# Kernel optimization log

Measured on AMD Instinct MI355X. Metric: run time of the kernel, lower is better.

Reference implementation:

```python
import jax, jax.numpy as jnp
import numpy as np

H, D = 8, 16
HD = H * D
SCALE0 = float(1.0 / np.sqrt(D * 1))   # degree-0 dot-product scale (order m=1)
SCALE1 = float(1.0 / np.sqrt(D * 3))   # degree-1 dot-product scale (order m=3)
SHARED = float(np.sqrt(0.5))           # shared_scale = sqrt(1/2) for DOT_PROD + SHARED
NEG = -1e9


def _split_heads_q(x):  # (b,n,HD,m) -> (b,H,n,D,m)
    b, n, _, m = x.shape
    return x.reshape(b, n, H, D, m).transpose(0, 2, 1, 3, 4)


def _split_heads_k(x):  # (b,n,N,HD,m) -> (b,H,n,N,D,m)
    b, n, N, _, m = x.shape
    return x.reshape(b, n, N, H, D, m).transpose(0, 3, 1, 2, 4, 5)


def _augment_kv(k, v, feats, W_self, null_k, null_v):
    # attend_self: VNLinear self key/value; use_null_kv: learned null tokens.
    b, n = feats.shape[:2]
    m = feats.shape[-1]
    skv = jnp.einsum('oc,bncm->bnom', W_self, feats)          # (b,n,2HD,m)
    sk, sv = jnp.split(skv, 2, axis=-2)
    sk = _split_heads_q(sk)[:, :, :, None]                     # (b,H,n,1,D,m)
    sv = _split_heads_q(sv)[:, :, :, None]
    nk = jnp.broadcast_to(null_k[None, :, None, None], (b, H, n, 1, D, m))
    nv = jnp.broadcast_to(null_v[None, :, None, None], (b, H, n, 1, D, m))
    k = jnp.concatenate([nk, sk, k], axis=3)                   # (b,H,n,2+N,D,m)
    v = jnp.concatenate([nv, sv, v], axis=3)
    return k, v


def _merge_heads(x):  # (b,H,n,D,m) -> (b,n,HD,m)
    b, _, n, _, m = x.shape
    return x.transpose(0, 2, 1, 3, 4).reshape(b, n, HD, m)


def _forward(q0, k0, v0, q1, k1, v1, feats0, feats1, edges,
             W_self_kv0, W_self_kv1, W_bias, self_bias, null_bias,
             null_k0, null_v0, null_k1, null_v1, head_weights1,
             W_out0, W_out1, neighbor_mask):
    b, n, N = edges.shape[:3]
    q0h, k0h, v0h = _split_heads_q(q0), _split_heads_k(k0), _split_heads_k(v0)
    q1h, k1h, v1h = _split_heads_q(q1), _split_heads_k(k1), _split_heads_k(v1)
    k0h, v0h = _augment_kv(k0h, v0h, feats0, W_self_kv0, null_k0, null_v0)
    k1h, v1h = _augment_kv(k1h, v1h, feats1, W_self_kv1, null_k1, null_v1)

    # pair bias for degree 0 (to_order==1); prepend null/self bias columns
    edge_bias = jnp.einsum('bnje,he->bhnj', edges, W_bias)     # (b,H,n,N)
    nb = jnp.broadcast_to(null_bias[None, :, None, None], (b, H, n, 1))
    sb = jnp.broadcast_to(self_bias[None, :, None, None], (b, H, n, 1))
    bias = jnp.concatenate([nb, sb, edge_bias], axis=-1)        # (b,H,n,2+N)

    sim0 = jnp.einsum('bhndm,bhnjdm->bhnj', q0h, k0h) * SCALE0 + bias
    w1 = jax.nn.softplus(head_weights1)                         # (1,H,1,1)
    sim1 = jnp.einsum('bhndm,bhnjdm->bhnj', q1h, k1h) * (SCALE1 * w1)

    total = (sim0 + sim1) * SHARED
    mask = jnp.concatenate(
        [jnp.ones((b, 1, n, 2), dtype=bool),                    # null + self always valid
         neighbor_mask[:, None]], axis=-1)
    total = jnp.where(mask, total, NEG)
    attn = jax.nn.softmax(total, axis=-1)                       # shared across degrees

    out0 = _merge_heads(jnp.einsum('bhnj,bhnjdm->bhndm', attn, v0h))
    out1 = _merge_heads(jnp.einsum('bhnj,bhnjdm->bhndm', attn, v1h))

    y0 = jnp.einsum('oc,bncm->bnom', W_out0, out0)              # FiberLinear deg 0
    y1 = jnp.einsum('oc,bncm->bnom', W_out1, out1)              # FiberLinear deg 1
    return y0, y1


def setup_inputs() -> dict:
    key = jax.random.key(0)
    ks = jax.random.split(key, 20)
    b, n, N, e = 1, 2048, 32, 32
    d0, d1 = 128, 64
    f = lambda k, s: jax.random.normal(k, s, dtype=jnp.float32) * 0.1
    return {
        'q0': f(ks[0], (b, n, HD, 1)), 'k0': f(ks[1], (b, n, N, HD, 1)), 'v0': f(ks[2], (b, n, N, HD, 1)),
        'q1': f(ks[3], (b, n, HD, 3)), 'k1': f(ks[4], (b, n, N, HD, 3)), 'v1': f(ks[5], (b, n, N, HD, 3)),
        'feats0': f(ks[6], (b, n, d0, 1)), 'feats1': f(ks[7], (b, n, d1, 3)),
        'edges': f(ks[8], (b, n, N, e)),
        'W_self_kv0': f(ks[9], (2 * HD, d0)), 'W_self_kv1': f(ks[10], (2 * HD, d1)),
        'W_bias': f(ks[11], (H, e)),
        'self_bias': jnp.zeros((H,), jnp.float32), 'null_bias': jnp.zeros((H,), jnp.float32),
        'null_k0': jnp.zeros((H, D, 1), jnp.float32), 'null_v0': jnp.zeros((H, D, 1), jnp.float32),
        'null_k1': jnp.zeros((H, D, 3), jnp.float32), 'null_v1': jnp.zeros((H, D, 3), jnp.float32),
        'head_weights1': jnp.full((1, H, 1, 1), float(np.log(np.e - 1.0)), jnp.float32),
        'W_out0': f(ks[12], (d0, HD)), 'W_out1': f(ks[13], (d1, HD)),
        'neighbor_mask': jax.random.uniform(ks[14], (b, n, N)) > 0.1,
    }


def reference(q0, k0, v0, q1, k1, v1, feats0, feats1, edges,
              W_self_kv0, W_self_kv1, W_bias, self_bias, null_bias,
              null_k0, null_v0, null_k1, null_v1, head_weights1,
              W_out0, W_out1, neighbor_mask):
    return _forward(q0, k0, v0, q1, k1, v1, feats0, feats1, edges,
                    W_self_kv0, W_self_kv1, W_bias, self_bias, null_bias,
                    null_k0, null_v0, null_k1, null_v1, head_weights1,
                    W_out0, W_out1, neighbor_mask)
```

## Files before the change

### kernel.cpp

```cpp
#include <hip/hip_runtime.h>

constexpr int kH  = 8;
constexpr int kD  = 16;
constexpr int kHD = 128;
constexpr int kN  = 32;
constexpr int kE  = 32;
constexpr int kD0 = 128;
constexpr int kD1 = 64;
constexpr int kPos = 2;

constexpr float SCALE0   = 0.25f;
constexpr float SCALE1   = 0.14433756729740643f;
constexpr float SHARED_S = 0.70710678118654752f;
constexpr float NEGV     = -1e9f;

__global__ __launch_bounds__(256, 4) void se3_fused(
    const float* __restrict__ q0, const float* __restrict__ q1,
    const float* __restrict__ k0, const float* __restrict__ k1,
    const float* __restrict__ v0, const float* __restrict__ v1,
    const float* __restrict__ feats0, const float* __restrict__ feats1,
    const float* __restrict__ edges,
    const float* __restrict__ Wskv0, const float* __restrict__ Wskv1,
    const float* __restrict__ Wbias,
    const float* __restrict__ sbias, const float* __restrict__ nbias,
    const float* __restrict__ nk0, const float* __restrict__ nk1,
    const float* __restrict__ nv0, const float* __restrict__ nv1,
    const float* __restrict__ hw1,
    const float* __restrict__ Wout0, const float* __restrict__ Wout1,
    const int* __restrict__ nmask,
    float* __restrict__ out, int n_total)
{
  const int i0 = blockIdx.x * kPos;
  const int t  = threadIdx.x;

  __shared__ __align__(16) float f0s[kPos][kD0];
  __shared__ __align__(16) float f1s[kPos][kD1 * 3];
  __shared__ __align__(16) float q0s[kPos][kHD];
  __shared__ __align__(16) float q1s[kPos][kHD * 3];
  __shared__ float edg[kPos][kN * (kE + 1)];
  __shared__ float wbs[kH * kE];
  __shared__ float w1s[kH];
  __shared__ int   nmL[kPos][kN];
  __shared__ float sk0[kPos][kHD];
  __shared__ __align__(16) float sk1[kPos][kHD * 3];
  __shared__ __align__(16) float sv0[kPos][kHD];
  __shared__ __align__(16) float sv1[kPos][kHD * 3];
  __shared__ float sc[kPos][kH][36];
  __shared__ __align__(16) float o0[kPos][kHD];
  __shared__ __align__(16) float o1[kPos][kHD * 3];

  if (t < kPos * 32) { int p = t >> 5, r = t & 31;
    ((float4*)f0s[p])[r] = ((const float4*)(feats0 + (size_t)(i0 + p) * kD0))[r]; }
  else if (t < kPos * 32 + kPos * 48) { int u = t - kPos * 32, p = u / 48, r = u % 48;
    ((float4*)f1s[p])[r] = ((const float4*)(feats1 + (size_t)(i0 + p) * kD1 * 3))[r]; }
  if (t >= 160 && t < 160 + kPos * 32) { int u = t - 160, p = u >> 5, r = u & 31;
    ((float4*)q0s[p])[r] = ((const float4*)(q0 + (size_t)(i0 + p) * kHD))[r]; }
  {
    int u = t; if (u < kPos * 96) { int p = u / 96, r = u % 96;
      ((float4*)q1s[p])[r] = ((const float4*)(q1 + (size_t)(i0 + p) * kHD * 3))[r]; }
  }
  for (int u = t; u < kPos * 256; u += 256) { int p = u >> 8, r = u & 255;
    float4 v = ((const float4*)(edges + (size_t)(i0 + p) * kN * kE))[r];
    int j = r >> 3, e4 = (r & 7) * 4;
    float* dst = &edg[p][j * 33 + e4];
    dst[0] = v.x; dst[1] = v.y; dst[2] = v.z; dst[3] = v.w; }
  if (t < kH * kE) wbs[t] = Wbias[t];
  if (t < kH) w1s[t] = log1pf(expf(hw1[t]));
  if (t < kPos * kN) { int p = t >> 5, j = t & 31;
    nmL[p][j] = nmask[(size_t)(i0 + p) * kN + j]; }
  __syncthreads();

  const int q4 = t & 3;
  const int qg = t >> 2;

  #pragma unroll
  for (int pass = 0; pass < 4; ++pass) {
    const int r = qg + 64 * pass;
    const float4* w0r = (const float4*)(Wskv0 + (size_t)r * kD0);
    float a0[kPos] = {};
    #pragma unroll
    for (int g = 0; g < 8; ++g) {
      float4 w = w0r[q4 + 4 * g]; int c = (q4 + 4 * g) * 4;
      #pragma unroll
      for (int p = 0; p < kPos; ++p)
        a0[p] += w.x * f0s[p][c] + w.y * f0s[p][c + 1]
               + w.z * f0s[p][c + 2] + w.w * f0s[p][c + 3];
    }
    const float4* w1r = (const float4*)(Wskv1 + (size_t)r * kD1);
    float a1[kPos][3] = {};
    #pragma unroll
    for (int g = 0; g < 4; ++g) {
      float4 w = w1r[q4 + 4 * g]; int c = (q4 + 4 * g) * 4;
      float wv[4] = {w.x, w.y, w.z, w.w};
      #pragma unroll
      for (int k = 0; k < 4; ++k) {
        #pragma unroll
        for (int p = 0; p < kPos; ++p) {
          const float* fp = &f1s[p][(c + k) * 3];
          a1[p][0] += wv[k] * fp[0];
          a1[p][1] += wv[k] * fp[1];
          a1[p][2] += wv[k] * fp[2];
        }
      }
    }
    #pragma unroll
    for (int p = 0; p < kPos; ++p) {
      a0[p] += __shfl_xor(a0[p], 1); a0[p] += __shfl_xor(a0[p], 2);
      #pragma unroll
      for (int c = 0; c < 3; ++c) {
        a1[p][c] += __shfl_xor(a1[p][c], 1);
        a1[p][c] += __shfl_xor(a1[p][c], 2);
      }
    }
    if (q4 == 0) {
      if (r < kHD) {
        #pragma unroll
        for (int p = 0; p < kPos; ++p) {
          sk0[p][r] = a0[p];
          sk1[p][r * 3 + 0] = a1[p][0];
          sk1[p][r * 3 + 1] = a1[p][1];
          sk1[p][r * 3 + 2] = a1[p][2];
        }
      } else {
        const int o = r - kHD;
        #pragma unroll
        for (int p = 0; p < kPos; ++p) {
          sv0[p][o] = a0[p];
          sv1[p][o * 3 + 0] = a1[p][0];
          sv1[p][o * 3 + 1] = a1[p][1];
          sv1[p][o * 3 + 2] = a1[p][2];
        }
      }
    }
  }
  __syncthreads();

  if (t < kPos * 16) {
    const int p = t >> 4, idx = t & 15;
    const int h = idx & 7;
    const bool is_self = idx >= 8;
    float s0 = 0.f, s1 = 0.f, bias;
    if (is_self) {
      #pragma unroll
      for (int d = 0; d < kD; ++d) s0 += q0s[p][h * kD + d] * sk0[p][h * kD + d];
      #pragma unroll
      for (int x = 0; x < 48; ++x) s1 += q1s[p][h * 48 + x] * sk1[p][h * 48 + x];
      bias = sbias[h];
    } else {
      #pragma unroll
      for (int d = 0; d < kD; ++d) s0 += q0s[p][h * kD + d] * nk0[h * kD + d];
      #pragma unroll
      for (int x = 0; x < 48; ++x) s1 += q1s[p][h * 48 + x] * nk1[h * 48 + x];
      bias = nbias[h];
    }
    sc[p][h][is_self ? 1 : 0] =
        (s0 * SCALE0 + bias + s1 * SCALE1 * w1s[h]) * SHARED_S;
  }

  {
    const int h  = qg & 7;
    const int jl = qg >> 3;
    const float w1h = w1s[h];
    float wbf[8];
    #pragma unroll
    for (int e = 0; e < 8; ++e) wbf[e] = wbs[h * kE + q4 * 8 + e];

    #pragma unroll
    for (int p = 0; p < kPos; ++p) {
      const int i = i0 + p;
      const float4 q0f = *((const float4*)(q0s[p] + h * kD) + q4);
      float4 q1f[3];
      #pragma unroll
      for (int pc = 0; pc < 3; ++pc)
        q1f[pc] = *((const float4*)(q1s[p] + h * 48 + pc * 16) + q4);

      const float* k0base = k0 + (size_t)i * kN * kHD + h * kD + q4 * 4;
      const float* k1base = k1 + (size_t)i * kN * kHD * 3 + h * 48 + q4 * 4;

      float4 kv0[4];
      float4 kv1[4][3];
      #pragma unroll
      for (int pp = 0; pp < 4; ++pp) {
        const int j = pp * 8 + jl;
        kv0[pp] = *((const float4*)(k0base + (size_t)j * kHD));
        #pragma unroll
        for (int pc = 0; pc < 3; ++pc)
          kv1[pp][pc] = *((const float4*)(k1base + (size_t)j * kHD * 3 + pc * 16));
      }

      #pragma unroll
      for (int pp = 0; pp < 4; ++pp) {
        const int j = pp * 8 + jl;
        float s0 = kv0[pp].x * q0f.x + kv0[pp].y * q0f.y
                 + kv0[pp].z * q0f.z + kv0[pp].w * q0f.w;
        float s1 = 0.f;
        #pragma unroll
        for (int pc = 0; pc < 3; ++pc)
          s1 += kv1[pp][pc].x * q1f[pc].x + kv1[pp][pc].y * q1f[pc].y
              + kv1[pp][pc].z * q1f[pc].z + kv1[pp][pc].w * q1f[pc].w;
        float bias = 0.f;
        #pragma unroll
        for (int e = 0; e < 8; ++e) bias += edg[p][j * 33 + q4 * 8 + e] * wbf[e];

        float part = s0 * SCALE0 + bias + s1 * SCALE1 * w1h;
        part += __shfl_xor(part, 1);
        part += __shfl_xor(part, 2);
        if (q4 == 0) sc[p][h][2 + j] = nmL[p][j] ? part * SHARED_S : NEGV;
      }
    }
  }
  __syncthreads();

  {
    const int row = t >> 4;
    const int p = row >> 3, h = row & 7, l = t & 15;
    float* rp = sc[p][h];
    float va = rp[2 + l], vb = rp[2 + l + 16];
    float mx = fmaxf(va, vb);
    #pragma unroll
    for (int off = 8; off > 0; off >>= 1) mx = fmaxf(mx, __shfl_xor(mx, off));
    float e0v = rp[0], e1v = rp[1];
    mx = fmaxf(mx, fmaxf(e0v, e1v));
    float ea = __expf(va - mx), eb = __expf(vb - mx);
    float sum = ea + eb;
    #pragma unroll
    for (int off = 8; off > 0; off >>= 1) sum += __shfl_xor(sum, off);
    float ee0 = __expf(e0v - mx), ee1 = __expf(e1v - mx);
    float inv = 1.f / (sum + ee0 + ee1);
    rp[2 + l] = ea * inv;
    rp[2 + l + 16] = eb * inv;
    if (l == 0) rp[0] = ee0 * inv;
    if (l == 1) rp[1] = ee1 * inv;
  }
  __syncthreads();

  {
    const int p = t >> 7, i = i0 + p;
    const int s = t & 127;
    float4 acc;
    if (s < 32) {
      const int h = s >> 2;
      const float* at = sc[p][h];
      float4 nv = ((const float4*)nv0)[s];
      float4 sv = ((const float4*)sv0[p])[s];
      acc.x = at[0] * nv.x + at[1] * sv.x;
      acc.y = at[0] * nv.y + at[1] * sv.y;
      acc.z = at[0] * nv.z + at[1] * sv.z;
      acc.w = at[0] * nv.w + at[1] * sv.w;
      const float4* vp = (const float4*)(v0 + (size_t)i * kN * kHD) + s;
      float4 vbuf[8];
      #pragma unroll
      for (int g = 0; g < 4; ++g) {
        #pragma unroll
        for (int r = 0; r < 8; ++r) vbuf[r] = vp[(g * 8 + r) * 32];
        #pragma unroll
        for (int r = 0; r < 8; ++r) {
          float a = at[2 + g * 8 + r];
          acc.x += a * vbuf[r].x; acc.y += a * vbuf[r].y;
          acc.z += a * vbuf[r].z; acc.w += a * vbuf[r].w;
        }
      }
      ((float4*)o0[p])[s] = acc;
    } else {
      const int s1 = s - 32;
      const int h = s1 / 12;
      const float* at = sc[p][h];
      float4 nv = ((const float4*)nv1)[s1];
      float4 sv = ((const float4*)sv1[p])[s1];
      acc.x = at[0] * nv.x + at[1] * sv.x;
      acc.y = at[0] * nv.y + at[1] * sv.y;
      acc.z = at[0] * nv.z + at[1] * sv.z;
      acc.w = at[0] * nv.w + at[1] * sv.w;
      const float4* vp = (const float4*)(v1 + (size_t)i * kN * kHD * 3) + s1;
      float4 vbuf[8];
      #pragma unroll
      for (int g = 0; g < 4; ++g) {
        #pragma unroll
        for (int r = 0; r < 8; ++r) vbuf[r] = vp[(g * 8 + r) * 96];
        #pragma unroll
        for (int r = 0; r < 8; ++r) {
          float a = at[2 + g * 8 + r];
          acc.x += a * vbuf[r].x; acc.y += a * vbuf[r].y;
          acc.z += a * vbuf[r].z; acc.w += a * vbuf[r].w;
        }
      }
      ((float4*)o1[p])[s1] = acc;
    }
  }
  __syncthreads();

  #pragma unroll
  for (int pass = 0; pass < 5; ++pass) {
    const int u = qg + 64 * pass;
    if (u < 128) {
      const float4* wr = (const float4*)(Wout0 + (size_t)u * kHD);
      float a[kPos] = {};
      #pragma unroll
      for (int g = 0; g < 8; ++g) {
        float4 w = wr[q4 + 4 * g]; int c = (q4 + 4 * g) * 4;
        #pragma unroll
        for (int p = 0; p < kPos; ++p)
          a[p] += w.x * o0[p][c] + w.y * o0[p][c + 1]
                + w.z * o0[p][c + 2] + w.w * o0[p][c + 3];
      }
      #pragma unroll
      for (int p = 0; p < kPos; ++p) {
        a[p] += __shfl_xor(a[p], 1); a[p] += __shfl_xor(a[p], 2);
      }
      if (q4 == 0) {
        #pragma unroll
        for (int p = 0; p < kPos; ++p)
          out[(size_t)(i0 + p) * kHD + u] = a[p];
      }
    } else {
      const int v2 = u - 128, o = v2 / 3, m = v2 - o * 3;
      const float4* wr = (const float4*)(Wout1 + (size_t)o * kHD);
      float a[kPos] = {};
      #pragma unroll
      for (int g = 0; g < 8; ++g) {
        float4 w = wr[q4 + 4 * g]; int c = (q4 + 4 * g) * 4;
        #pragma unroll
        for (int p = 0; p < kPos; ++p)
          a[p] += w.x * o1[p][(c + 0) * 3 + m] + w.y * o1[p][(c + 1) * 3 + m]
                + w.z * o1[p][(c + 2) * 3 + m] + w.w * o1[p][(c + 3) * 3 + m];
      }
      #pragma unroll
      for (int p = 0; p < kPos; ++p) {
        a[p] += __shfl_xor(a[p], 1); a[p] += __shfl_xor(a[p], 2);
      }
      if (q4 == 0) {
        #pragma unroll
        for (int p = 0; p < kPos; ++p)
          out[(size_t)n_total * kHD + (size_t)(i0 + p) * 192 + v2] = a[p];
      }
    }
  }
}

extern "C" void kernel_launch(void* const* d_in, const int* in_sizes, int n_in,
                              void* d_out, int out_size, void* d_ws, size_t ws_size,
                              hipStream_t stream) {
  const int n = in_sizes[0] / kHD;
  const float* q0     = (const float*)d_in[0];
  const float* k0     = (const float*)d_in[1];
  const float* v0     = (const float*)d_in[2];
  const float* q1     = (const float*)d_in[3];
  const float* k1     = (const float*)d_in[4];
  const float* v1     = (const float*)d_in[5];
  const float* feats0 = (const float*)d_in[6];
  const float* feats1 = (const float*)d_in[7];
  const float* edges  = (const float*)d_in[8];
  const float* Wskv0  = (const float*)d_in[9];
  const float* Wskv1  = (const float*)d_in[10];
  const float* Wbias  = (const float*)d_in[11];
  const float* sbias  = (const float*)d_in[12];
  const float* nbias  = (const float*)d_in[13];
  const float* nk0    = (const float*)d_in[14];
  const float* nv0    = (const float*)d_in[15];
  const float* nk1    = (const float*)d_in[16];
  const float* nv1    = (const float*)d_in[17];
  const float* hw1    = (const float*)d_in[18];
  const float* Wout0  = (const float*)d_in[19];
  const float* Wout1  = (const float*)d_in[20];
  const int*   nmask  = (const int*)d_in[21];

  se3_fused<<<n / kPos, 256, 0, stream>>>(
      q0, q1, k0, k1, v0, v1, feats0, feats1, edges,
      Wskv0, Wskv1, Wbias, sbias, nbias, nk0, nk1, nv0, nv1, hw1,
      Wout0, Wout1, nmask, (float*)d_out, n);
}
```

Baseline: 324.6 us.

## Process one position per block, prefetch keys early, split value reduction across halves

The kernel now handles one node per block instead of two, doubling the grid. Key loads for the attention scores are issued at kernel start, before the shared-memory staging and the self-KV projection, so their latency overlaps other work. The value aggregation is split across both halves of the block (each covering half the neighbors), and an extra reduction pass plus barrier combines the two partial sums. In exchange, the weight-matrix reads (Wskv, Wout) are amortized over only one position per block, so weight traffic per node doubles.

```diff
diff --git a/kernel.cpp b/kernel.cpp
--- a/kernel.cpp
+++ b/kernel.cpp
@@ -7,7 +7,6 @@
 constexpr int kE  = 32;
 constexpr int kD0 = 128;
 constexpr int kD1 = 64;
-constexpr int kPos = 2;
 
 constexpr float SCALE0   = 0.25f;
 constexpr float SCALE1   = 0.14433756729740643f;
@@ -30,191 +29,166 @@
     const int* __restrict__ nmask,
     float* __restrict__ out, int n_total)
 {
-  const int i0 = blockIdx.x * kPos;
-  const int t  = threadIdx.x;
-
-  __shared__ __align__(16) float f0s[kPos][kD0];
-  __shared__ __align__(16) float f1s[kPos][kD1 * 3];
-  __shared__ __align__(16) float q0s[kPos][kHD];
-  __shared__ __align__(16) float q1s[kPos][kHD * 3];
-  __shared__ float edg[kPos][kN * (kE + 1)];
+  const int i = blockIdx.x;
+  const int t = threadIdx.x;
+  const int q4 = t & 3;
+  const int qg = t >> 2;
+  const int hB = qg & 7;
+  const int jl = qg >> 3;
+
+  __shared__ __align__(16) float f0s[kD0];
+  __shared__ __align__(16) float f1s[kD1 * 3];
+  __shared__ __align__(16) float q0s[kHD];
+  __shared__ __align__(16) float q1s[kHD * 3];
+  __shared__ float edg[kN * (kE + 1)];
   __shared__ float wbs[kH * kE];
   __shared__ float w1s[kH];
-  __shared__ int   nmL[kPos][kN];
-  __shared__ float sk0[kPos][kHD];
-  __shared__ __align__(16) float sk1[kPos][kHD * 3];
-  __shared__ __align__(16) float sv0[kPos][kHD];
-  __shared__ __align__(16) float sv1[kPos][kHD * 3];
-  __shared__ float sc[kPos][kH][36];
-  __shared__ __align__(16) float o0[kPos][kHD];
-  __shared__ __align__(16) float o1[kPos][kHD * 3];
-
-  if (t < kPos * 32) { int p = t >> 5, r = t & 31;
-    ((float4*)f0s[p])[r] = ((const float4*)(feats0 + (size_t)(i0 + p) * kD0))[r]; }
-  else if (t < kPos * 32 + kPos * 48) { int u = t - kPos * 32, p = u / 48, r = u % 48;
-    ((float4*)f1s[p])[r] = ((const float4*)(feats1 + (size_t)(i0 + p) * kD1 * 3))[r]; }
-  if (t >= 160 && t < 160 + kPos * 32) { int u = t - 160, p = u >> 5, r = u & 31;
-    ((float4*)q0s[p])[r] = ((const float4*)(q0 + (size_t)(i0 + p) * kHD))[r]; }
-  {
-    int u = t; if (u < kPos * 96) { int p = u / 96, r = u % 96;
-      ((float4*)q1s[p])[r] = ((const float4*)(q1 + (size_t)(i0 + p) * kHD * 3))[r]; }
-  }
-  for (int u = t; u < kPos * 256; u += 256) { int p = u >> 8, r = u & 255;
-    float4 v = ((const float4*)(edges + (size_t)(i0 + p) * kN * kE))[r];
-    int j = r >> 3, e4 = (r & 7) * 4;
-    float* dst = &edg[p][j * 33 + e4];
-    dst[0] = v.x; dst[1] = v.y; dst[2] = v.z; dst[3] = v.w; }
-  if (t < kH * kE) wbs[t] = Wbias[t];
-  if (t < kH) w1s[t] = log1pf(expf(hw1[t]));
-  if (t < kPos * kN) { int p = t >> 5, j = t & 31;
-    nmL[p][j] = nmask[(size_t)(i0 + p) * kN + j]; }
-  __syncthreads();
-
-  const int q4 = t & 3;
-  const int qg = t >> 2;
+  __shared__ int   nmL[kN];
+  __shared__ float sk0[kHD];
+  __shared__ __align__(16) float sk1[kHD * 3];
+  __shared__ __align__(16) float sv0[kHD];
+  __shared__ __align__(16) float sv1[kHD * 3];
+  __shared__ float sc[kH][36];
+  __shared__ __align__(16) float o0p[2][kHD];
+  __shared__ __align__(16) float o1p[2][kHD * 3];
+
+  float4 fqv = {0.f, 0.f, 0.f, 0.f};
+  if (t < 32)        fqv = ((const float4*)(feats0 + (size_t)i * kD0))[t];
+  else if (t < 80)   fqv = ((const float4*)(feats1 + (size_t)i * kD1 * 3))[t - 32];
+  else if (t < 112)  fqv = ((const float4*)(q0 + (size_t)i * kHD))[t - 80];
+  else if (t < 208)  fqv = ((const float4*)(q1 + (size_t)i * kHD * 3))[t - 112];
+  float4 ev = ((const float4*)(edges + (size_t)i * kN * kE))[t];
+  float wv  = Wbias[t];
+  int   nmv = (t < kN) ? nmask[(size_t)i * kN + t] : 0;
+  float hv  = (t < kH) ? hw1[t] : 0.f;
+
+  const float* k0base = k0 + (size_t)i * kN * kHD + hB * kD + q4 * 4;
+  const float* k1base = k1 + (size_t)i * kN * kHD * 3 + hB * 48 + q4 * 4;
+  float4 kv0[4];
+  float4 kv1[4][3];
+  #pragma unroll
+  for (int pp = 0; pp < 4; ++pp) {
+    const int j = pp * 8 + jl;
+    kv0[pp] = *((const float4*)(k0base + (size_t)j * kHD));
+    #pragma unroll
+    for (int pc = 0; pc < 3; ++pc)
+      kv1[pp][pc] = *((const float4*)(k1base + (size_t)j * kHD * 3 + pc * 16));
+  }
+  __builtin_amdgcn_sched_barrier(0);
+
+  if (t < 32)        ((float4*)f0s)[t] = fqv;
+  else if (t < 80)   ((float4*)f1s)[t - 32] = fqv;
+  else if (t < 112)  ((float4*)q0s)[t - 80] = fqv;
+  else if (t < 208)  ((float4*)q1s)[t - 112] = fqv;
+  { int j = t >> 3, e4 = (t & 7) * 4;
+    float* dst = &edg[j * 33 + e4];
+    dst[0] = ev.x; dst[1] = ev.y; dst[2] = ev.z; dst[3] = ev.w; }
+  wbs[t] = wv;
+  if (t < kN) nmL[t] = nmv;
+  if (t < kH) w1s[t] = log1pf(expf(hv));
+  __syncthreads();
 
   #pragma unroll
   for (int pass = 0; pass < 4; ++pass) {
     const int r = qg + 64 * pass;
     const float4* w0r = (const float4*)(Wskv0 + (size_t)r * kD0);
-    float a0[kPos] = {};
+    float a0 = 0.f;
     #pragma unroll
     for (int g = 0; g < 8; ++g) {
       float4 w = w0r[q4 + 4 * g]; int c = (q4 + 4 * g) * 4;
-      #pragma unroll
-      for (int p = 0; p < kPos; ++p)
-        a0[p] += w.x * f0s[p][c] + w.y * f0s[p][c + 1]
-               + w.z * f0s[p][c + 2] + w.w * f0s[p][c + 3];
+      a0 += w.x * f0s[c] + w.y * f0s[c + 1]
+          + w.z * f0s[c + 2] + w.w * f0s[c + 3];
     }
     const float4* w1r = (const float4*)(Wskv1 + (size_t)r * kD1);
-    float a1[kPos][3] = {};
+    float a1[3] = {};
     #pragma unroll
     for (int g = 0; g < 4; ++g) {
       float4 w = w1r[q4 + 4 * g]; int c = (q4 + 4 * g) * 4;
-      float wv[4] = {w.x, w.y, w.z, w.w};
+      float wvv[4] = {w.x, w.y, w.z, w.w};
       #pragma unroll
       for (int k = 0; k < 4; ++k) {
-        #pragma unroll
-        for (int p = 0; p < kPos; ++p) {
-          const float* fp = &f1s[p][(c + k) * 3];
-          a1[p][0] += wv[k] * fp[0];
-          a1[p][1] += wv[k] * fp[1];
-          a1[p][2] += wv[k] * fp[2];
-        }
-      }
-    }
-    #pragma unroll
-    for (int p = 0; p < kPos; ++p) {
-      a0[p] += __shfl_xor(a0[p], 1); a0[p] += __shfl_xor(a0[p], 2);
-      #pragma unroll
-      for (int c = 0; c < 3; ++c) {
-        a1[p][c] += __shfl_xor(a1[p][c], 1);
-        a1[p][c] += __shfl_xor(a1[p][c], 2);
-      }
+        const float* fp = &f1s[(c + k) * 3];
+        a1[0] += wvv[k] * fp[0];
+        a1[1] += wvv[k] * fp[1];
+        a1[2] += wvv[k] * fp[2];
+      }
+    }
+    a0 += __shfl_xor(a0, 1); a0 += __shfl_xor(a0, 2);
+    #pragma unroll
+    for (int c = 0; c < 3; ++c) {
+      a1[c] += __shfl_xor(a1[c], 1);
+      a1[c] += __shfl_xor(a1[c], 2);
     }
     if (q4 == 0) {
       if (r < kHD) {
-        #pragma unroll
-        for (int p = 0; p < kPos; ++p) {
-          sk0[p][r] = a0[p];
-          sk1[p][r * 3 + 0] = a1[p][0];
-          sk1[p][r * 3 + 1] = a1[p][1];
-          sk1[p][r * 3 + 2] = a1[p][2];
-        }
+        sk0[r] = a0;
+        sk1[r * 3 + 0] = a1[0]; sk1[r * 3 + 1] = a1[1]; sk1[r * 3 + 2] = a1[2];
       } else {
         const int o = r - kHD;
-        #pragma unroll
-        for (int p = 0; p < kPos; ++p) {
-          sv0[p][o] = a0[p];
-          sv1[p][o * 3 + 0] = a1[p][0];
-          sv1[p][o * 3 + 1] = a1[p][1];
-          sv1[p][o * 3 + 2] = a1[p][2];
-        }
-      }
-    }
-  }
-  __syncthreads();
-
-  if (t < kPos * 16) {
-    const int p = t >> 4, idx = t & 15;
-    const int h = idx & 7;
-    const bool is_self = idx >= 8;
+        sv0[o] = a0;
+        sv1[o * 3 + 0] = a1[0]; sv1[o * 3 + 1] = a1[1]; sv1[o * 3 + 2] = a1[2];
+      }
+    }
+  }
+  __syncthreads();
+
+  if (t < 16) {
+    const int h = t & 7;
+    const bool is_self = t >= 8;
     float s0 = 0.f, s1 = 0.f, bias;
     if (is_self) {
       #pragma unroll
-      for (int d = 0; d < kD; ++d) s0 += q0s[p][h * kD + d] * sk0[p][h * kD + d];
-      #pragma unroll
-      for (int x = 0; x < 48; ++x) s1 += q1s[p][h * 48 + x] * sk1[p][h * 48 + x];
+      for (int d = 0; d < kD; ++d) s0 += q0s[h * kD + d] * sk0[h * kD + d];
+      #pragma unroll
+      for (int x = 0; x < 48; ++x) s1 += q1s[h * 48 + x] * sk1[h * 48 + x];
       bias = sbias[h];
     } else {
       #pragma unroll
-      for (int d = 0; d < kD; ++d) s0 += q0s[p][h * kD + d] * nk0[h * kD + d];
-      #pragma unroll
-      for (int x = 0; x < 48; ++x) s1 += q1s[p][h * 48 + x] * nk1[h * 48 + x];
+      for (int d = 0; d < kD; ++d) s0 += q0s[h * kD + d] * nk0[h * kD + d];
+      #pragma unroll
+      for (int x = 0; x < 48; ++x) s1 += q1s[h * 48 + x] * nk1[h * 48 + x];
       bias = nbias[h];
     }
-    sc[p][h][is_self ? 1 : 0] =
+    sc[h][is_self ? 1 : 0] =
         (s0 * SCALE0 + bias + s1 * SCALE1 * w1s[h]) * SHARED_S;
   }
 
   {
-    const int h  = qg & 7;
-    const int jl = qg >> 3;
-    const float w1h = w1s[h];
+    const float w1h = w1s[hB];
     float wbf[8];
     #pragma unroll
-    for (int e = 0; e < 8; ++e) wbf[e] = wbs[h * kE + q4 * 8 + e];
-
-    #pragma unroll
-    for (int p = 0; p < kPos; ++p) {
-      const int i = i0 + p;
-      const float4 q0f = *((const float4*)(q0s[p] + h * kD) + q4);
-      float4 q1f[3];
+    for (int e = 0; e < 8; ++e) wbf[e] = wbs[hB * kE + q4 * 8 + e];
+    const float4 q0f = *((const float4*)(q0s + hB * kD) + q4);
+    float4 q1f[3];
+    #pragma unroll
+    for (int pc = 0; pc < 3; ++pc)
+      q1f[pc] = *((const float4*)(q1s + hB * 48 + pc * 16) + q4);
+
+    #pragma unroll
+    for (int pp = 0; pp < 4; ++pp) {
+      const int j = pp * 8 + jl;
+      float s0 = kv0[pp].x * q0f.x + kv0[pp].y * q0f.y
+               + kv0[pp].z * q0f.z + kv0[pp].w * q0f.w;
+      float s1 = 0.f;
       #pragma unroll
       for (int pc = 0; pc < 3; ++pc)
-        q1f[pc] = *((const float4*)(q1s[p] + h * 48 + pc * 16) + q4);
-
-      const float* k0base = k0 + (size_t)i * kN * kHD + h * kD + q4 * 4;
-      const float* k1base = k1 + (size_t)i * kN * kHD * 3 + h * 48 + q4 * 4;
-
-      float4 kv0[4];
-      float4 kv1[4][3];
-      #pragma unroll
-      for (int pp = 0; pp < 4; ++pp) {
-        const int j = pp * 8 + jl;
-        kv0[pp] = *((const float4*)(k0base + (size_t)j * kHD));
-        #pragma unroll
-        for (int pc = 0; pc < 3; ++pc)
-          kv1[pp][pc] = *((const float4*)(k1base + (size_t)j * kHD * 3 + pc * 16));
-      }
-
-      #pragma unroll
-      for (int pp = 0; pp < 4; ++pp) {
-        const int j = pp * 8 + jl;
-        float s0 = kv0[pp].x * q0f.x + kv0[pp].y * q0f.y
-                 + kv0[pp].z * q0f.z + kv0[pp].w * q0f.w;
-        float s1 = 0.f;
-        #pragma unroll
-        for (int pc = 0; pc < 3; ++pc)
-          s1 += kv1[pp][pc].x * q1f[pc].x + kv1[pp][pc].y * q1f[pc].y
-              + kv1[pp][pc].z * q1f[pc].z + kv1[pp][pc].w * q1f[pc].w;
-        float bias = 0.f;
-        #pragma unroll
-        for (int e = 0; e < 8; ++e) bias += edg[p][j * 33 + q4 * 8 + e] * wbf[e];
-
-        float part = s0 * SCALE0 + bias + s1 * SCALE1 * w1h;
-        part += __shfl_xor(part, 1);
-        part += __shfl_xor(part, 2);
-        if (q4 == 0) sc[p][h][2 + j] = nmL[p][j] ? part * SHARED_S : NEGV;
-      }
-    }
-  }
-  __syncthreads();
-
-  {
-    const int row = t >> 4;
-    const int p = row >> 3, h = row & 7, l = t & 15;
-    float* rp = sc[p][h];
+        s1 += kv1[pp][pc].x * q1f[pc].x + kv1[pp][pc].y * q1f[pc].y
+            + kv1[pp][pc].z * q1f[pc].z + kv1[pp][pc].w * q1f[pc].w;
+      float bias = 0.f;
+      #pragma unroll
+      for (int e = 0; e < 8; ++e) bias += edg[j * 33 + q4 * 8 + e] * wbf[e];
+
+      float part = s0 * SCALE0 + bias + s1 * SCALE1 * w1h;
+      part += __shfl_xor(part, 1);
+      part += __shfl_xor(part, 2);
+      if (q4 == 0) sc[hB][2 + j] = nmL[j] ? part * SHARED_S : NEGV;
+    }
+  }
+  __syncthreads();
+
+  if (t < 128) {
+    const int h = t >> 4, l = t & 15;
+    float* rp = sc[h];
     float va = rp[2 + l], vb = rp[2 + l + 16];
     float mx = fmaxf(va, vb);
     #pragma unroll
@@ -235,22 +209,25 @@
   __syncthreads();
 
   {
-    const int p = t >> 7, i = i0 + p;
+    const int halfD = t >> 7;
     const int s = t & 127;
-    float4 acc;
+    float4 acc = {0.f, 0.f, 0.f, 0.f};
     if (s < 32) {
       const int h = s >> 2;
-      const float* at = sc[p][h];
-      float4 nv = ((const float4*)nv0)[s];
-      float4 sv = ((const float4*)sv0[p])[s];
-      acc.x = at[0] * nv.x + at[1] * sv.x;
-      acc.y = at[0] * nv.y + at[1] * sv.y;
-      acc.z = at[0] * nv.z + at[1] * sv.z;
-      acc.w = at[0] * nv.w + at[1] * sv.w;
+      const float* at = sc[h];
+      if (halfD == 0) {
+        float4 nv = ((const float4*)nv0)[s];
+        float4 sv = ((const float4*)sv0)[s];
+        acc.x = at[0] * nv.x + at[1] * sv.x;
+        acc.y = at[0] * nv.y + at[1] * sv.y;
+        acc.z = at[0] * nv.z + at[1] * sv.z;
+        acc.w = at[0] * nv.w + at[1] * sv.w;
+      }
       const float4* vp = (const float4*)(v0 + (size_t)i * kN * kHD) + s;
       float4 vbuf[8];
       #pragma unroll
-      for (int g = 0; g < 4; ++g) {
+      for (int gg = 0; gg < 2; ++gg) {
+        const int g = halfD * 2 + gg;
         #pragma unroll
         for (int r = 0; r < 8; ++r) vbuf[r] = vp[(g * 8 + r) * 32];
         #pragma unroll
@@ -260,21 +237,24 @@
           acc.z += a * vbuf[r].z; acc.w += a * vbuf[r].w;
         }
       }
-      ((float4*)o0[p])[s] = acc;
+      ((float4*)o0p[halfD])[s] = acc;
     } else {
       const int s1 = s - 32;
       const int h = s1 / 12;
-      const float* at = sc[p][h];
-      float4 nv = ((const float4*)nv1)[s1];
-      float4 sv = ((const float4*)sv1[p])[s1];
-      acc.x = at[0] * nv.x + at[1] * sv.x;
-      acc.y = at[0] * nv.y + at[1] * sv.y;
-      acc.z = at[0] * nv.z + at[1] * sv.z;
-      acc.w = at[0] * nv.w + at[1] * sv.w;
+      const float* at = sc[h];
+      if (halfD == 0) {
+        float4 nv = ((const float4*)nv1)[s1];
+        float4 sv = ((const float4*)sv1)[s1];
+        acc.x = at[0] * nv.x + at[1] * sv.x;
+        acc.y = at[0] * nv.y + at[1] * sv.y;
+        acc.z = at[0] * nv.z + at[1] * sv.z;
+        acc.w = at[0] * nv.w + at[1] * sv.w;
+      }
       const float4* vp = (const float4*)(v1 + (size_t)i * kN * kHD * 3) + s1;
       float4 vbuf[8];
       #pragma unroll
-      for (int g = 0; g < 4; ++g) {
+      for (int gg = 0; gg < 2; ++gg) {
+        const int g = halfD * 2 + gg;
         #pragma unroll
         for (int r = 0; r < 8; ++r) vbuf[r] = vp[(g * 8 + r) * 96];
         #pragma unroll
@@ -284,7 +264,21 @@
           acc.z += a * vbuf[r].z; acc.w += a * vbuf[r].w;
         }
       }
-      ((float4*)o1[p])[s1] = acc;
+      ((float4*)o1p[halfD])[s1] = acc;
+    }
+  }
+  __syncthreads();
+
+  if (t < 128) {
+    if (t < 32) {
+      float4 a = ((float4*)o0p[0])[t], b = ((float4*)o0p[1])[t];
+      a.x += b.x; a.y += b.y; a.z += b.z; a.w += b.w;
+      ((float4*)o0p[0])[t] = a;
+    } else {
+      const int s1 = t - 32;
+      float4 a = ((float4*)o1p[0])[s1], b = ((float4*)o1p[1])[s1];
+      a.x += b.x; a.y += b.y; a.z += b.z; a.w += b.w;
+      ((float4*)o1p[0])[s1] = a;
     }
   }
   __syncthreads();
@@ -294,45 +288,28 @@
     const int u = qg + 64 * pass;
     if (u < 128) {
       const float4* wr = (const float4*)(Wout0 + (size_t)u * kHD);
-      float a[kPos] = {};
+      float a = 0.f;
       #pragma unroll
       for (int g = 0; g < 8; ++g) {
         float4 w = wr[q4 + 4 * g]; int c = (q4 + 4 * g) * 4;
-        #pragma unroll
-        for (int p = 0; p < kPos; ++p)
-          a[p] += w.x * o0[p][c] + w.y * o0[p][c + 1]
-                + w.z * o0[p][c + 2] + w.w * o0[p][c + 3];
-      }
-      #pragma unroll
-      for (int p = 0; p < kPos; ++p) {
-        a[p] += __shfl_xor(a[p], 1); a[p] += __shfl_xor(a[p], 2);
-      }
-      if (q4 == 0) {
-        #pragma unroll
-        for (int p = 0; p < kPos; ++p)
-          out[(size_t)(i0 + p) * kHD + u] = a[p];
-      }
+        a += w.x * o0p[0][c] + w.y * o0p[0][c + 1]
+           + w.z * o0p[0][c + 2] + w.w * o0p[0][c + 3];
+      }
+      a += __shfl_xor(a, 1); a += __shfl_xor(a, 2);
+      if (q4 == 0) out[(size_t)i * kHD + u] = a;
     } else {
       const int v2 = u - 128, o = v2 / 3, m = v2 - o * 3;
       const float4* wr = (const float4*)(Wout1 + (size_t)o * kHD);
-      float a[kPos] = {};
+      float a = 0.f;
       #pragma unroll
       for (int g = 0; g < 8; ++g) {
         float4 w = wr[q4 + 4 * g]; int c = (q4 + 4 * g) * 4;
-        #pragma unroll
-        for (int p = 0; p < kPos; ++p)
-          a[p] += w.x * o1[p][(c + 0) * 3 + m] + w.y * o1[p][(c + 1) * 3 + m]
-                + w.z * o1[p][(c + 2) * 3 + m] + w.w * o1[p][(c + 3) * 3 + m];
-      }
-      #pragma unroll
-      for (int p = 0; p < kPos; ++p) {
-        a[p] += __shfl_xor(a[p], 1); a[p] += __shfl_xor(a[p], 2);
-      }
-      if (q4 == 0) {
-        #pragma unroll
-        for (int p = 0; p < kPos; ++p)
-          out[(size_t)n_total * kHD + (size_t)(i0 + p) * 192 + v2] = a[p];
-      }
+        a += w.x * o1p[0][(c + 0) * 3 + m] + w.y * o1p[0][(c + 1) * 3 + m]
+           + w.z * o1p[0][(c + 2) * 3 + m] + w.w * o1p[0][(c + 3) * 3 + m];
+      }
+      a += __shfl_xor(a, 1); a += __shfl_xor(a, 2);
+      if (q4 == 0)
+        out[(size_t)n_total * kHD + (size_t)i * 192 + v2] = a;
     }
   }
 }
@@ -364,7 +341,7 @@
   const float* Wout1  = (const float*)d_in[20];
   const int*   nmask  = (const int*)d_in[21];
 
-  se3_fused<<<n / kPos, 256, 0, stream>>>(
+  se3_fused<<<n, 256, 0, stream>>>(
       q0, q1, k0, k1, v0, v1, feats0, feats1, edges,
       Wskv0, Wskv1, Wbias, sbias, nbias, nk0, nk1, nv0, nv1, hw1,
       Wout0, Wout1, nmask, (float*)d_out, n);
```

Result: slower. 356.6 us (+9.9%).
